# Optimization experiments

Measured on AMD Instinct MI355X. Metric: run time of the kernel, lower is better.

## Reference

```python
import jax, jax.numpy as jnp
import numpy as np

N0, N1, N2 = 80000, 40000, 20000
E1, E2 = 500000, 250000
FIN = 128        # in_channels
H = 2            # heads
C1 = 64          # hidden_channels -> layer1 out per head (concat -> 128)
C2 = 64          # out_channels -> layer2 out per head (mean over heads)
ED = 10          # edge_dim per embedding, total edge feat = 2*ED = 20
NTYPE, NTS = 23, 1158


def setup_inputs() -> dict:
    key = jax.random.key(0)
    ks = jax.random.split(key, 48)
    sc = 0.05
    inp = {
        "x": jax.random.normal(ks[0], (N0, FIN), jnp.float32),
        "ei1_src": jax.random.randint(ks[1], (E1,), 0, N0),
        "ei1_dst": jax.random.randint(ks[2], (E1,), 0, N1),
        "et1": jax.random.randint(ks[3], (E1,), 0, NTYPE),
        "ets1": jax.random.randint(ks[4], (E1,), 0, NTS),
        "ei2_src": jax.random.randint(ks[5], (E2,), 0, N1),
        "ei2_dst": jax.random.randint(ks[6], (E2,), 0, N2),
        "et2": jax.random.randint(ks[7], (E2,), 0, NTYPE),
        "ets2": jax.random.randint(ks[8], (E2,), 0, NTS),
        # shared edge embeddings (Linear(23,10), Linear(1158,10))
        "edge_W": jax.random.normal(ks[9], (ED, NTYPE), jnp.float32) * sc,
        "edge_b": jax.random.normal(ks[10], (ED,), jnp.float32) * sc,
        "time_W": jax.random.normal(ks[11], (ED, NTS), jnp.float32) * sc,
        "time_b": jax.random.normal(ks[12], (ED,), jnp.float32) * sc,
    }
    # layer 1: in=128, heads=2, C=64, concat=True (out dim 128)
    hc1 = H * C1
    inp["Wq1"] = jax.random.normal(ks[13], (hc1, FIN), jnp.float32) * sc
    inp["bq1"] = jnp.zeros((hc1,), jnp.float32)
    inp["Wk1"] = jax.random.normal(ks[14], (hc1, FIN), jnp.float32) * sc
    inp["bk1"] = jnp.zeros((hc1,), jnp.float32)
    inp["Wv1"] = jax.random.normal(ks[15], (hc1, FIN), jnp.float32) * sc
    inp["bv1"] = jnp.zeros((hc1,), jnp.float32)
    inp["We1"] = jax.random.normal(ks[16], (hc1, 2 * ED), jnp.float32) * sc
    inp["Wskip1"] = jax.random.normal(ks[17], (hc1, FIN), jnp.float32) * sc
    inp["bskip1"] = jnp.zeros((hc1,), jnp.float32)
    inp["Wbeta1"] = jax.random.normal(ks[18], (1, 3 * hc1), jnp.float32) * sc
    inp["ln_g"] = jnp.ones((hc1,), jnp.float32)
    inp["ln_b"] = jnp.zeros((hc1,), jnp.float32)
    # layer 2: in=128, heads=2, C=64, concat=False (out dim 64)
    hc2 = H * C2
    inp["Wq2"] = jax.random.normal(ks[19], (hc2, hc1), jnp.float32) * sc
    inp["bq2"] = jnp.zeros((hc2,), jnp.float32)
    inp["Wk2"] = jax.random.normal(ks[20], (hc2, hc1), jnp.float32) * sc
    inp["bk2"] = jnp.zeros((hc2,), jnp.float32)
    inp["Wv2"] = jax.random.normal(ks[21], (hc2, hc1), jnp.float32) * sc
    inp["bv2"] = jnp.zeros((hc2,), jnp.float32)
    inp["We2"] = jax.random.normal(ks[22], (hc2, 2 * ED), jnp.float32) * sc
    inp["Wskip2"] = jax.random.normal(ks[23], (C2, hc1), jnp.float32) * sc
    inp["bskip2"] = jnp.zeros((C2,), jnp.float32)
    inp["Wbeta2"] = jax.random.normal(ks[24], (1, 3 * C2), jnp.float32) * sc
    return inp


def _edge_feat(et, ets, edge_W, edge_b, time_W, time_b):
    # one_hot(e) @ W.T + b == W.T[e] + b (avoids materializing huge one-hot)
    return jnp.concatenate([jnp.take(edge_W.T, et, axis=0) + edge_b,
                            jnp.take(time_W.T, ets, axis=0) + time_b], axis=-1)


def _conv(x_src, x_dst, src, dst, ef, Wq, bq, Wk, bk, Wv, bv, We,
          Wskip, bskip, Wbeta, concat):
    n_dst = x_dst.shape[0]
    HC = Wq.shape[0]
    C = HC // H
    q = (x_dst @ Wq.T + bq).reshape(n_dst, H, C)            # [Nd,H,C]
    k = (x_src @ Wk.T + bk)[src].reshape(-1, H, C)          # [E,H,C]
    v = (x_src @ Wv.T + bv)[src].reshape(-1, H, C)
    e = (ef @ We.T).reshape(-1, H, C)
    k = k + e
    alpha = jnp.einsum('ehc,ehc->eh', q[dst], k) / np.sqrt(C).astype(np.float32)
    # segment softmax over destination nodes
    m = jax.ops.segment_max(alpha, dst, num_segments=n_dst)
    ex = jnp.exp(alpha - m[dst])
    s = jax.ops.segment_sum(ex, dst, num_segments=n_dst)
    a = ex / (s[dst] + 1e-16)                               # [E,H]
    msg = (v + e) * a[..., None]                            # [E,H,C]
    out = jax.ops.segment_sum(msg.reshape(-1, HC), dst, num_segments=n_dst)
    out = out if concat else out.reshape(n_dst, H, C).mean(axis=1)
    x_r = x_dst @ Wskip.T + bskip
    beta = jax.nn.sigmoid(
        jnp.concatenate([out, x_r, out - x_r], axis=-1) @ Wbeta.T)  # [Nd,1]
    return beta * x_r + (1.0 - beta) * out


def _layernorm(x, g, b):
    mu = x.mean(-1, keepdims=True)
    var = x.var(-1, keepdims=True)
    return (x - mu) / jnp.sqrt(var + 1e-5) * g + b


def reference(x, ei1_src, ei1_dst, et1, ets1, ei2_src, ei2_dst, et2, ets2,
              edge_W, edge_b, time_W, time_b,
              Wq1, bq1, Wk1, bk1, Wv1, bv1, We1, Wskip1, bskip1, Wbeta1,
              ln_g, ln_b,
              Wq2, bq2, Wk2, bk2, Wv2, bv2, We2, Wskip2, bskip2, Wbeta2):
    ef1 = _edge_feat(et1, ets1, edge_W, edge_b, time_W, time_b)
    h = _conv(x, x[:N1], ei1_src, ei1_dst, ef1,
              Wq1, bq1, Wk1, bk1, Wv1, bv1, We1, Wskip1, bskip1, Wbeta1,
              concat=True)
    h = jax.nn.gelu(_layernorm(h, ln_g, ln_b), approximate=False)
    ef2 = _edge_feat(et2, ets2, edge_W, edge_b, time_W, time_b)
    o = _conv(h, h[:N2], ei2_src, ei2_dst, ef2,
              Wq2, bq2, Wk2, bk2, Wv2, bv2, We2, Wskip2, bskip2, Wbeta2,
              concat=False)
    return jax.nn.log_softmax(o, axis=-1)
```

## Files before the change

kernel.cpp:

```cpp
#include <hip/hip_runtime.h>
#include <math.h>

#define N0 80000
#define N1 40000
#define N2 20000
#define E1C 500000
#define E2C 250000
#define NTYPE 23
#define NTS 1158

#define NB1 157
#define NB2 79
#define KV1B 1250
#define QR1B 625
#define CNTB 2930
#define KV2B 625
#define QR2B 313
#define FILLB 2930

#define OFF_XB    0u
#define OFF_QR1   5120000u
#define OFF_KV1   15360000u
#define OFF_H     25600000u
#define OFF_QR2   28160000u
#define OFF_KV2   32000000u
#define OFF_WB1   37120000u
#define OFF_BP1   37160000u
#define OFF_WB2   37170000u
#define OFF_BP2   37200000u
#define OFF_TA1   37210000u
#define OFF_TB1   37213000u
#define OFF_TA2   37370000u
#define OFF_TB2   37373000u
#define OFF_RP1   37530000u
#define OFF_CUR1  37580000u
#define OFF_EIX1  37630000u
#define OFF_BS1   38140000u
#define OFF_RP2   38150000u
#define OFF_CUR2  38180000u
#define OFF_EIX2  38210000u
#define OFF_BS2   38470000u
#define OFF_DONE  38480000u

typedef __bf16 bf16x8 __attribute__((ext_vector_type(8)));
typedef float f32x4 __attribute__((ext_vector_type(4)));

static __device__ __forceinline__ float b2f(unsigned short u) {
    union { unsigned int i; float f; } c;
    c.i = ((unsigned int)u) << 16;
    return c.f;
}
static __device__ __forceinline__ unsigned short f2b(float f) {
    unsigned int u = __float_as_uint(f);
    unsigned int r = (u + 0x7fffu + ((u >> 16) & 1u)) >> 16;
    return (unsigned short)r;
}
static __device__ __forceinline__ bf16x8 ldfrag(const unsigned short* p) {
    return *reinterpret_cast<const bf16x8*>(p);
}

template <int CTRL>
static __device__ __forceinline__ float dpp_addstep(float v) {
    int x = __builtin_amdgcn_mov_dpp(__float_as_int(v), CTRL, 0xF, 0xF, true);
    return v + __int_as_float(x);
}
static __device__ __forceinline__ float red16(float v) {
    v = dpp_addstep<0xB1>(v);
    v = dpp_addstep<0x4E>(v);
    v = dpp_addstep<0x141>(v);
    v = dpp_addstep<0x140>(v);
    return v;
}
template <int CTRL>
static __device__ __forceinline__ float dpp_maxstep(float v) {
    int x = __builtin_amdgcn_mov_dpp(__float_as_int(v), CTRL, 0xF, 0xF, true);
    return fmaxf(v, __int_as_float(x));
}
static __device__ __forceinline__ float red16max(float v) {
    v = dpp_maxstep<0xB1>(v);
    v = dpp_maxstep<0x4E>(v);
    v = dpp_maxstep<0x141>(v);
    v = dpp_maxstep<0x140>(v);
    return v;
}

#define LDSS 136

template <int NTILES>
static __device__ __forceinline__ void dev_gemm_bf16out(
    const unsigned short* __restrict__ XB, const unsigned short* __restrict__ WB,
    const float* __restrict__ BP, unsigned short* __restrict__ Y, int n, int blk,
    unsigned short* sb) {
    constexpr int COLS = NTILES * 16;
    constexpr int HALF = NTILES / 2;
    constexpr int HCOLS = HALF * 16;
    int wave = threadIdx.x >> 6, lane = threadIdx.x & 63;
    int m = lane & 15, quad = lane >> 4;
    int rowbase = blk * 64 + wave * 16;
    int arow = rowbase + m; if (arow >= n) arow = n - 1;
    unsigned short* swave = sb + wave * 16 * LDSS;
    const unsigned short* xrow = XB + (size_t)arow * 128 + quad * 8;
    bf16x8 a0 = ldfrag(xrow), a1 = ldfrag(xrow + 32);
    bf16x8 a2 = ldfrag(xrow + 64), a3 = ldfrag(xrow + 96);
    f32x4 acc[NTILES];
#pragma unroll
    for (int t = 0; t < NTILES; t++) acc[t] = (f32x4){0.f, 0.f, 0.f, 0.f};
#pragma unroll
    for (int t = 0; t < NTILES; t++) {
        const unsigned short* wt = WB + (size_t)t * 2048 + lane * 8;
        acc[t] = __builtin_amdgcn_mfma_f32_16x16x32_bf16(a0, ldfrag(wt), acc[t], 0, 0, 0);
        acc[t] = __builtin_amdgcn_mfma_f32_16x16x32_bf16(a1, ldfrag(wt + 512), acc[t], 0, 0, 0);
        acc[t] = __builtin_amdgcn_mfma_f32_16x16x32_bf16(a2, ldfrag(wt + 1024), acc[t], 0, 0, 0);
        acc[t] = __builtin_amdgcn_mfma_f32_16x16x32_bf16(a3, ldfrag(wt + 1536), acc[t], 0, 0, 0);
    }
    int tswz_bit = (quad >> 1) & 1;
#pragma unroll
    for (int half = 0; half < 2; half++) {
#pragma unroll
        for (int t = 0; t < HALF; t++) {
            int tt = half * HALF + t;
            int tsw = t ^ tswz_bit;
            float b = BP[tt * 16 + m];
#pragma unroll
            for (int r = 0; r < 4; r++)
                swave[(quad * 4 + r) * LDSS + tsw * 16 + m] = f2b(acc[tt][r] + b);
        }
#pragma unroll
        for (int i = 0; i < 4; i++) {
            int idx = i * 64 + lane;
            int r = idx / (HCOLS / 8), g = idx % (HCOLS / 8);
            int gs = g ^ (((r >> 3) & 1) << 1);
            int grow = rowbase + r;
            if (grow < n) {
                uint4 v = *(const uint4*)&swave[r * LDSS + gs * 8];
                *(uint4*)(Y + (size_t)grow * COLS + half * HCOLS + g * 8) = v;
            }
        }
    }
}

template <int NTILES>
static __device__ __forceinline__ void dev_gemm_f32out(
    const unsigned short* __restrict__ XB, const unsigned short* __restrict__ WB,
    const float* __restrict__ BP, float* __restrict__ Y, int n, int blk) {
    constexpr int COLS = NTILES * 16;
    int wave = threadIdx.x >> 6, lane = threadIdx.x & 63;
    int m = lane & 15, quad = lane >> 4;
    int rowbase = blk * 64 + wave * 16;
    int arow = rowbase + m; if (arow >= n) arow = n - 1;
    const unsigned short* xrow = XB + (size_t)arow * 128 + quad * 8;
    bf16x8 a0 = ldfrag(xrow), a1 = ldfrag(xrow + 32);
    bf16x8 a2 = ldfrag(xrow + 64), a3 = ldfrag(xrow + 96);
    f32x4 acc[NTILES];
#pragma unroll
    for (int t = 0; t < NTILES; t++) acc[t] = (f32x4){0.f, 0.f, 0.f, 0.f};
#pragma unroll
    for (int t = 0; t < NTILES; t++) {
        const unsigned short* wt = WB + (size_t)t * 2048 + lane * 8;
        acc[t] = __builtin_amdgcn_mfma_f32_16x16x32_bf16(a0, ldfrag(wt), acc[t], 0, 0, 0);
        acc[t] = __builtin_amdgcn_mfma_f32_16x16x32_bf16(a1, ldfrag(wt + 512), acc[t], 0, 0, 0);
        acc[t] = __builtin_amdgcn_mfma_f32_16x16x32_bf16(a2, ldfrag(wt + 1024), acc[t], 0, 0, 0);
        acc[t] = __builtin_amdgcn_mfma_f32_16x16x32_bf16(a3, ldfrag(wt + 1536), acc[t], 0, 0, 0);
    }
#pragma unroll
    for (int t = 0; t < NTILES; t++) {
        float b = BP[t * 16 + m];
#pragma unroll
        for (int r = 0; r < 4; r++) {
            int grow = rowbase + quad * 4 + r;
            if (grow < n) Y[(size_t)grow * COLS + t * 16 + m] = acc[t][r] + b;
        }
    }
}

__global__ __launch_bounds__(256) void prep(
    const float* __restrict__ x, unsigned short* __restrict__ XB,
    const float* __restrict__ Wk1, const float* __restrict__ Wv1,
    const float* __restrict__ Wq1, const float* __restrict__ Wskip1,
    const float* __restrict__ bk1, const float* __restrict__ bv1,
    const float* __restrict__ bq1, const float* __restrict__ bskip1,
    const float* __restrict__ Wk2, const float* __restrict__ Wv2,
    const float* __restrict__ Wq2, const float* __restrict__ Wskip2,
    const float* __restrict__ bk2, const float* __restrict__ bv2,
    const float* __restrict__ bq2, const float* __restrict__ bskip2,
    unsigned short* __restrict__ WB1, float* __restrict__ BP1,
    unsigned short* __restrict__ WB2, float* __restrict__ BP2,
    const float* __restrict__ edge_W, const float* __restrict__ edge_b,
    const float* __restrict__ time_W, const float* __restrict__ time_b,
    const float* __restrict__ We1, const float* __restrict__ We2,
    float* __restrict__ TA1, float* __restrict__ TB1,
    float* __restrict__ TA2, float* __restrict__ TB2,
    int* __restrict__ cnt1, int* __restrict__ cnt2, int* __restrict__ done) {
    int tid = blockIdx.x * blockDim.x + threadIdx.x;
    int stride = gridDim.x * blockDim.x;
    for (int i = tid; i < N0 * 32; i += stride) {
        float4 v = *(const float4*)(x + (size_t)i * 4);
        ushort4 u;
        u.x = f2b(v.x); u.y = f2b(v.y); u.z = f2b(v.z); u.w = f2b(v.w);
        *(ushort4*)(XB + (size_t)i * 4) = u;
    }
    for (int i = tid; i < 512 * 128; i += stride) {
        int j = i & 7, l = (i >> 3) & 63, ks = (i >> 9) & 3, t = i >> 11;
        int row = t * 16 + (l & 15);
        int col = ks * 32 + ((l >> 4) & 3) * 8 + j;
        const float* w; int off;
        if (row < 128) { w = Wk1; off = 0; }
        else if (row < 256) { w = Wv1; off = 128; }
        else if (row < 384) { w = Wq1; off = 256; }
        else { w = Wskip1; off = 384; }
        WB1[i] = f2b(w[(size_t)(row - off) * 128 + col]);
    }
    for (int i = tid; i < 512; i += stride) {
        const float* b; int off;
        if (i < 128) { b = bk1; off = 0; }
        else if (i < 256) { b = bv1; off = 128; }
        else if (i < 384) { b = bq1; off = 256; }
        else { b = bskip1; off = 384; }
        BP1[i] = b[i - off];
    }
    for (int i = tid; i < 448 * 128; i += stride) {
        int j = i & 7, l = (i >> 3) & 63, ks = (i >> 9) & 3, t = i >> 11;
        int row = t * 16 + (l & 15);
        int col = ks * 32 + ((l >> 4) & 3) * 8 + j;
        const float* w; int off;
        if (row < 128) { w = Wk2; off = 0; }
        else if (row < 256) { w = Wv2; off = 128; }
        else if (row < 384) { w = Wq2; off = 256; }
        else { w = Wskip2; off = 384; }
        WB2[i] = f2b(w[(size_t)(row - off) * 128 + col]);
    }
    for (int i = tid; i < 448; i += stride) {
        const float* b; int off;
        if (i < 128) { b = bk2; off = 0; }
        else if (i < 256) { b = bv2; off = 128; }
        else if (i < 384) { b = bq2; off = 256; }
        else { b = bskip2; off = 384; }
        BP2[i] = b[i - off];
    }
    const int TBL = (NTYPE + NTS) * 128;
    for (int i = tid; i < TBL; i += stride) {
        if (i < NTYPE * 128) {
            int e = i >> 7, c = i & 127;
            float s1 = 0.f, s2 = 0.f;
#pragma unroll
            for (int j = 0; j < 10; j++) {
                float fj = edge_W[j * NTYPE + e] + edge_b[j];
                s1 += fj * We1[c * 20 + j];
                s2 += fj * We2[c * 20 + j];
            }
            TA1[i] = s1; TA2[i] = s2;
        } else {
            int u = i - NTYPE * 128;
            int ts = u >> 7, c = u & 127;
            float s1 = 0.f, s2 = 0.f;
#pragma unroll
            for (int j = 0; j < 10; j++) {
                float fj = time_W[j * NTS + ts] + time_b[j];
                s1 += fj * We1[c * 20 + 10 + j];
                s2 += fj * We2[c * 20 + 10 + j];
            }
            TB1[u] = s1; TB2[u] = s2;
        }
    }
    for (int i = tid; i < N1 + N2 + 1; i += stride) {
        if (i < N1) cnt1[i] = 0;
        else if (i < N1 + N2) cnt2[i - N1] = 0;
        else *done = 0;
    }
}

__global__ __launch_bounds__(256) void mega_l1(
    const unsigned short* __restrict__ XB,
    const unsigned short* __restrict__ WB1, const float* __restrict__ BP1,
    unsigned short* __restrict__ KV1, float* __restrict__ QR1,
    const int* __restrict__ d1, const int* __restrict__ d2,
    int* __restrict__ cnt1, int* __restrict__ cnt2) {
    __shared__ unsigned short sbuf[4 * 16 * LDSS];
    int b = blockIdx.x;
    if (b < KV1B) {
        dev_gemm_bf16out<16>(XB, WB1, BP1, KV1, N0, b, sbuf);
    } else if (b < KV1B + QR1B) {
        dev_gemm_f32out<16>(XB, WB1 + 256 * 128, BP1 + 256, QR1, N1, b - KV1B);
    } else {
        int t = (b - KV1B - QR1B) * 256 + threadIdx.x;
        if (t < E1C) atomicAdd(&cnt1[d1[t]], 1);
        else {
            t -= E1C;
            if (t < E2C) atomicAdd(&cnt2[d2[t]], 1);
        }
    }
}

__global__ __launch_bounds__(256) void gemm_l2(
    const unsigned short* __restrict__ H,
    const unsigned short* __restrict__ WB2, const float* __restrict__ BP2,
    unsigned short* __restrict__ KV2, float* __restrict__ QR2) {
    __shared__ unsigned short sbuf[4 * 16 * LDSS];
    int b = blockIdx.x;
    if (b < KV2B) dev_gemm_bf16out<16>(H, WB2, BP2, KV2, N1, b, sbuf);
    else dev_gemm_f32out<12>(H, WB2 + 256 * 128, BP2 + 256, QR2, N2, b - KV2B);
}

__global__ __launch_bounds__(256) void bsum_scan(
    const int* __restrict__ cnt1, int* __restrict__ bs1,
    const int* __restrict__ cnt2, int* __restrict__ bs2, int* __restrict__ done) {
    __shared__ int s[256];
    __shared__ int amlast;
    int b = blockIdx.x;
    const int* cnt; int* bs; int n, lb;
    if (b < NB1) { cnt = cnt1; bs = bs1; n = N1; lb = b; }
    else { cnt = cnt2; bs = bs2; n = N2; lb = b - NB1; }
    int t = lb * 256 + threadIdx.x;
    s[threadIdx.x] = (t < n) ? cnt[t] : 0;
    __syncthreads();
    for (int off = 128; off; off >>= 1) {
        if (threadIdx.x < off) s[threadIdx.x] += s[threadIdx.x + off];
        __syncthreads();
    }
    if (threadIdx.x == 0) {
        atomicExch(&bs[lb], s[0]);
        __threadfence();
        int prev = atomicAdd(done, 1);
        amlast = (prev == NB1 + NB2 - 1) ? 1 : 0;
    }
    __syncthreads();
    if (!amlast) return;
    int tt = threadIdx.x;
    int v1 = (tt < NB1) ? atomicAdd(&bs1[tt], 0) : 0;
    s[tt] = v1;
    __syncthreads();
    for (int off = 1; off < 256; off <<= 1) {
        int u = (tt >= off) ? s[tt - off] : 0;
        __syncthreads();
        s[tt] += u;
        __syncthreads();
    }
    if (tt < NB1) bs1[tt] = s[tt] - v1;
    __syncthreads();
    int v2 = (tt < NB2) ? atomicAdd(&bs2[tt], 0) : 0;
    s[tt] = v2;
    __syncthreads();
    for (int off = 1; off < 256; off <<= 1) {
        int u = (tt >= off) ? s[tt - off] : 0;
        __syncthreads();
        s[tt] += u;
        __syncthreads();
    }
    if (tt < NB2) bs2[tt] = s[tt] - v2;
}

__global__ __launch_bounds__(256) void bscan_both(
    int* __restrict__ cnt1, const int* __restrict__ bs1, int* __restrict__ rp1,
    int* __restrict__ cnt2, const int* __restrict__ bs2, int* __restrict__ rp2) {
    __shared__ int s[256];
    int b = blockIdx.x;
    int* cnt; const int* bs; int* rp; int n, lb;
    if (b < NB1) { cnt = cnt1; bs = bs1; rp = rp1; n = N1; lb = b; }
    else { cnt = cnt2; bs = bs2; rp = rp2; n = N2; lb = b - NB1; }
    int t = lb * 256 + threadIdx.x;
    int v = (t < n) ? cnt[t] : 0;
    if (t < n) cnt[t] = 0;
    s[threadIdx.x] = v;
    __syncthreads();
    for (int off = 1; off < 256; off <<= 1) {
        int u = (threadIdx.x >= off) ? s[threadIdx.x - off] : 0;
        __syncthreads();
        s[threadIdx.x] += u;
        __syncthreads();
    }
    int incl = s[threadIdx.x];
    int base = bs[lb];
    if (t < n) rp[t] = base + incl - v;
    if (t == n - 1) rp[n] = base + incl;
}

__global__ __launch_bounds__(256) void fill_both(
    const int* __restrict__ d1, const int* __restrict__ rp1,
    int* __restrict__ cur1, int* __restrict__ eix1,
    const int* __restrict__ d2, const int* __restrict__ rp2,
    int* __restrict__ cur2, int* __restrict__ eix2) {
    int t = blockIdx.x * 256 + threadIdx.x;
    if (t < E1C) {
        int d = d1[t];
        eix1[rp1[d] + atomicAdd(&cur1[d], 1)] = t;
    } else {
        t -= E1C;
        if (t < E2C) {
            int d = d2[t];
            eix2[rp2[d] + atomicAdd(&cur2[d], 1)] = t;
        }
    }
}

__global__ __launch_bounds__(256) void agg_layer1(
    const int* __restrict__ rowptr, const int* __restrict__ eidx,
    const int* __restrict__ src, const int* __restrict__ et, const int* __restrict__ ets,
    const float* __restrict__ TA, const float* __restrict__ TB,
    const float* __restrict__ QR, const unsigned short* __restrict__ KV,
    const float* __restrict__ Wbeta,
    const float* __restrict__ ln_g, const float* __restrict__ ln_b,
    unsigned short* __restrict__ hout, int n) {
    int wid = (blockIdx.x * blockDim.x + threadIdx.x) >> 6;
    int lane = threadIdx.x & 63;
    if (wid >= n) return;
    int s = lane >> 5, cg = lane & 15;
    int co = ((lane >> 4) & 1) * 64 + 4 * cg;
    int beg = rowptr[wid], end = rowptr[wid + 1];
    float4 q4 = *(const float4*)(QR + (size_t)wid * 256 + co);
    float ax = 0.f, ay = 0.f, az = 0.f, aw = 0.f, suma = 0.f;
    int p = beg + s;
    if (p < end) {
        int e0 = eidx[p];
        int sn0 = src[e0], t0 = et[e0], ts0 = ets[e0];
        int p1 = p + 2;
        bool m1 = p1 < end;
        int e1 = eidx[m1 ? p1 : beg];
        int sn1 = src[e1], t1 = et[e1], ts1 = ets[e1];
        float4 ta0 = *(const float4*)(TA + t0 * 128 + co);
        float4 tb0 = *(const float4*)(TB + ts0 * 128 + co);
        const unsigned short* kv0 = KV + (size_t)sn0 * 256;
        ushort4 ku0 = *(const ushort4*)(kv0 + co);
        ushort4 vu0 = *(const ushort4*)(kv0 + 128 + co);
        for (;;) {
            int p2 = p1 + 2;
            bool m2 = p2 < end;
            int e2 = eidx[m2 ? p2 : beg];
            int sn2 = src[e2], t2 = et[e2], ts2 = ets[e2];
            float4 ta1 = *(const float4*)(TA + t1 * 128 + co);
            float4 tb1 = *(const float4*)(TB + ts1 * 128 + co);
            const unsigned short* kv1 = KV + (size_t)sn1 * 256;
            ushort4 ku1 = *(const ushort4*)(kv1 + co);
            ushort4 vu1 = *(const ushort4*)(kv1 + 128 + co);
            float e0c = ta0.x + tb0.x, e1c = ta0.y + tb0.y;
            float e2c = ta0.z + tb0.z, e3c = ta0.w + tb0.w;
            float pp = q4.x * (b2f(ku0.x) + e0c) + q4.y * (b2f(ku0.y) + e1c)
                     + q4.z * (b2f(ku0.z) + e2c) + q4.w * (b2f(ku0.w) + e3c);
            pp = red16(pp);
            float a = __expf(pp * 0.125f);
            ax += a * (b2f(vu0.x) + e0c); ay += a * (b2f(vu0.y) + e1c);
            az += a * (b2f(vu0.z) + e2c); aw += a * (b2f(vu0.w) + e3c);
            suma += a;
            if (!m1) break;
            p1 = p2; m1 = m2;
            sn1 = sn2; t1 = t2; ts1 = ts2;
            ta0 = ta1; tb0 = tb1; ku0 = ku1; vu0 = vu1;
        }
    }
    ax += __shfl_xor(ax, 32); ay += __shfl_xor(ay, 32);
    az += __shfl_xor(az, 32); aw += __shfl_xor(aw, 32);
    suma += __shfl_xor(suma, 32);
    float inv_s = 1.f / (suma + 1e-16f);
    float ox = ax * inv_s, oy = ay * inv_s, oz = az * inv_s, ow = aw * inv_s;
    float4 r4 = *(const float4*)(QR + (size_t)wid * 256 + 128 + co);
    float4 wo = *(const float4*)(Wbeta + co);
    float4 wr = *(const float4*)(Wbeta + 128 + co);
    float4 wd = *(const float4*)(Wbeta + 256 + co);
    float pb = wo.x * ox + wr.x * r4.x + wd.x * (ox - r4.x)
             + wo.y * oy + wr.y * r4.y + wd.y * (oy - r4.y)
             + wo.z * oz + wr.z * r4.z + wd.z * (oz - r4.z)
             + wo.w * ow + wr.w * r4.w + wd.w * (ow - r4.w);
    pb = red16(pb);
    pb += __shfl_xor(pb, 16);
    float beta = 1.f / (1.f + __expf(-pb));
    float gx = beta * r4.x + (1.f - beta) * ox;
    float gy = beta * r4.y + (1.f - beta) * oy;
    float gz = beta * r4.z + (1.f - beta) * oz;
    float gw = beta * r4.w + (1.f - beta) * ow;
    float sm = gx + gy + gz + gw;
    float sq = gx * gx + gy * gy + gz * gz + gw * gw;
    sm = red16(sm); sm += __shfl_xor(sm, 16);
    sq = red16(sq); sq += __shfl_xor(sq, 16);
    float mu = sm * (1.f / 128.f);
    float var = sq * (1.f / 128.f) - mu * mu;
    float inv = rsqrtf(var + 1e-5f);
    float4 lg = *(const float4*)(ln_g + co);
    float4 lb = *(const float4*)(ln_b + co);
    float yx = (gx - mu) * inv * lg.x + lb.x;
    float yy = (gy - mu) * inv * lg.y + lb.y;
    float yz = (gz - mu) * inv * lg.z + lb.z;
    float yw = (gw - mu) * inv * lg.w + lb.w;
    const float ISQ2 = 0.70710678118654752f;
    yx = 0.5f * yx * (1.f + erff(yx * ISQ2));
    yy = 0.5f * yy * (1.f + erff(yy * ISQ2));
    yz = 0.5f * yz * (1.f + erff(yz * ISQ2));
    yw = 0.5f * yw * (1.f + erff(yw * ISQ2));
    if (s == 0) {
        ushort4 hv;
        hv.x = f2b(yx); hv.y = f2b(yy); hv.z = f2b(yz); hv.w = f2b(yw);
        *(ushort4*)(hout + (size_t)wid * 128 + co) = hv;
    }
}

__global__ __launch_bounds__(256) void agg_layer2(
    const int* __restrict__ rowptr, const int* __restrict__ eidx,
    const int* __restrict__ src, const int* __restrict__ et, const int* __restrict__ ets,
    const float* __restrict__ TA, const float* __restrict__ TB,
    const float* __restrict__ QR, const unsigned short* __restrict__ KV,
    const float* __restrict__ Wbeta,
    float* __restrict__ o, int n) {
    int wid = (blockIdx.x * blockDim.x + threadIdx.x) >> 6;
    int lane = threadIdx.x & 63;
    if (wid >= n) return;
    int s = lane >> 5, cg = lane & 15;
    int co = ((lane >> 4) & 1) * 64 + 4 * cg;
    int beg = rowptr[wid], end = rowptr[wid + 1];
    float4 q4 = *(const float4*)(QR + (size_t)wid * 192 + co);
    float ax = 0.f, ay = 0.f, az = 0.f, aw = 0.f, suma = 0.f;
    int p = beg + s;
    if (p < end) {
        int e0 = eidx[p];
        int sn0 = src[e0], t0 = et[e0], ts0 = ets[e0];
        int p1 = p + 2;
        bool m1 = p1 < end;
        int e1 = eidx[m1 ? p1 : beg];
        int sn1 = src[e1], t1 = et[e1], ts1 = ets[e1];
        float4 ta0 = *(const float4*)(TA + t0 * 128 + co);
        float4 tb0 = *(const float4*)(TB + ts0 * 128 + co);
        const unsigned short* kv0 = KV + (size_t)sn0 * 256;
        ushort4 ku0 = *(const ushort4*)(kv0 + co);
        ushort4 vu0 = *(const ushort4*)(kv0 + 128 + co);
        for (;;) {
            int p2 = p1 + 2;
            bool m2 = p2 < end;
            int e2 = eidx[m2 ? p2 : beg];
            int sn2 = src[e2], t2 = et[e2], ts2 = ets[e2];
            float4 ta1 = *(const float4*)(TA + t1 * 128 + co);
            float4 tb1 = *(const float4*)(TB + ts1 * 128 + co);
            const unsigned short* kv1 = KV + (size_t)sn1 * 256;
            ushort4 ku1 = *(const ushort4*)(kv1 + co);
            ushort4 vu1 = *(const ushort4*)(kv1 + 128 + co);
            float e0c = ta0.x + tb0.x, e1c = ta0.y + tb0.y;
            float e2c = ta0.z + tb0.z, e3c = ta0.w + tb0.w;
            float pp = q4.x * (b2f(ku0.x) + e0c) + q4.y * (b2f(ku0.y) + e1c)
                     + q4.z * (b2f(ku0.z) + e2c) + q4.w * (b2f(ku0.w) + e3c);
            pp = red16(pp);
            float a = __expf(pp * 0.125f);
            ax += a * (b2f(vu0.x) + e0c); ay += a * (b2f(vu0.y) + e1c);
            az += a * (b2f(vu0.z) + e2c); aw += a * (b2f(vu0.w) + e3c);
            suma += a;
            if (!m1) break;
            p1 = p2; m1 = m2;
            sn1 = sn2; t1 = t2; ts1 = ts2;
            ta0 = ta1; tb0 = tb1; ku0 = ku1; vu0 = vu1;
        }
    }
    ax += __shfl_xor(ax, 32); ay += __shfl_xor(ay, 32);
    az += __shfl_xor(az, 32); aw += __shfl_xor(aw, 32);
    suma += __shfl_xor(suma, 32);
    float inv_s = 1.f / (suma + 1e-16f);
    float ox = ax * inv_s, oy = ay * inv_s, oz = az * inv_s, ow = aw * inv_s;
    ox = 0.5f * (ox + __shfl_xor(ox, 16));
    oy = 0.5f * (oy + __shfl_xor(oy, 16));
    oz = 0.5f * (oz + __shfl_xor(oz, 16));
    ow = 0.5f * (ow + __shfl_xor(ow, 16));
    float4 r4 = *(const float4*)(QR + (size_t)wid * 192 + 128 + 4 * cg);
    float4 wo = *(const float4*)(Wbeta + 4 * cg);
    float4 wr = *(const float4*)(Wbeta + 64 + 4 * cg);
    float4 wd = *(const float4*)(Wbeta + 128 + 4 * cg);
    float pb = wo.x * ox + wr.x * r4.x + wd.x * (ox - r4.x)
             + wo.y * oy + wr.y * r4.y + wd.y * (oy - r4.y)
             + wo.z * oz + wr.z * r4.z + wd.z * (oz - r4.z)
             + wo.w * ow + wr.w * r4.w + wd.w * (ow - r4.w);
    pb = red16(pb);
    float beta = 1.f / (1.f + __expf(-pb));
    float vx = beta * r4.x + (1.f - beta) * ox;
    float vy = beta * r4.y + (1.f - beta) * oy;
    float vz = beta * r4.z + (1.f - beta) * oz;
    float vw = beta * r4.w + (1.f - beta) * ow;
    float m = fmaxf(fmaxf(vx, vy), fmaxf(vz, vw));
    m = red16max(m);
    float se = __expf(vx - m) + __expf(vy - m) + __expf(vz - m) + __expf(vw - m);
    se = red16(se);
    float lse = m + logf(se);
    if (lane < 16)
        *(float4*)(o + (size_t)wid * 64 + 4 * cg) =
            make_float4(vx - lse, vy - lse, vz - lse, vw - lse);
}

extern "C" void kernel_launch(void* const* d_in, const int* in_sizes, int n_in,
                              void* d_out, int out_size, void* d_ws, size_t ws_size,
                              hipStream_t stream) {
    const float* x        = (const float*)d_in[0];
    const int*   ei1_src  = (const int*)d_in[1];
    const int*   ei1_dst  = (const int*)d_in[2];
    const int*   et1      = (const int*)d_in[3];
    const int*   ets1     = (const int*)d_in[4];
    const int*   ei2_src  = (const int*)d_in[5];
    const int*   ei2_dst  = (const int*)d_in[6];
    const int*   et2      = (const int*)d_in[7];
    const int*   ets2     = (const int*)d_in[8];
    const float* edge_W   = (const float*)d_in[9];
    const float* edge_b   = (const float*)d_in[10];
    const float* time_W   = (const float*)d_in[11];
    const float* time_b   = (const float*)d_in[12];
    const float* Wq1      = (const float*)d_in[13];
    const float* bq1      = (const float*)d_in[14];
    const float* Wk1      = (const float*)d_in[15];
    const float* bk1      = (const float*)d_in[16];
    const float* Wv1      = (const float*)d_in[17];
    const float* bv1      = (const float*)d_in[18];
    const float* We1      = (const float*)d_in[19];
    const float* Wskip1   = (const float*)d_in[20];
    const float* bskip1   = (const float*)d_in[21];
    const float* Wbeta1   = (const float*)d_in[22];
    const float* ln_g     = (const float*)d_in[23];
    const float* ln_b     = (const float*)d_in[24];
    const float* Wq2      = (const float*)d_in[25];
    const float* bq2      = (const float*)d_in[26];
    const float* Wk2      = (const float*)d_in[27];
    const float* bk2      = (const float*)d_in[28];
    const float* Wv2      = (const float*)d_in[29];
    const float* bv2      = (const float*)d_in[30];
    const float* We2      = (const float*)d_in[31];
    const float* Wskip2   = (const float*)d_in[32];
    const float* bskip2   = (const float*)d_in[33];
    const float* Wbeta2   = (const float*)d_in[34];

    float* ws = (float*)d_ws;
    unsigned short* xb  = (unsigned short*)(ws + OFF_XB);
    float* qr1          = ws + OFF_QR1;
    unsigned short* kv1 = (unsigned short*)(ws + OFF_KV1);
    unsigned short* h   = (unsigned short*)(ws + OFF_H);
    float* qr2          = ws + OFF_QR2;
    unsigned short* kv2 = (unsigned short*)(ws + OFF_KV2);
    unsigned short* wb1 = (unsigned short*)(ws + OFF_WB1);
    float* bp1          = ws + OFF_BP1;
    unsigned short* wb2 = (unsigned short*)(ws + OFF_WB2);
    float* bp2          = ws + OFF_BP2;
    float* ta1          = ws + OFF_TA1;
    float* tb1          = ws + OFF_TB1;
    float* ta2          = ws + OFF_TA2;
    float* tb2          = ws + OFF_TB2;
    int*   rp1          = (int*)(ws + OFF_RP1);
    int*   cur1         = (int*)(ws + OFF_CUR1);
    int*   eix1         = (int*)(ws + OFF_EIX1);
    int*   bs1          = (int*)(ws + OFF_BS1);
    int*   rp2          = (int*)(ws + OFF_RP2);
    int*   cur2         = (int*)(ws + OFF_CUR2);
    int*   eix2         = (int*)(ws + OFF_EIX2);
    int*   bs2          = (int*)(ws + OFF_BS2);
    int*   done         = (int*)(ws + OFF_DONE);

    prep<<<2048, 256, 0, stream>>>(
        x, xb,
        Wk1, Wv1, Wq1, Wskip1, bk1, bv1, bq1, bskip1,
        Wk2, Wv2, Wq2, Wskip2, bk2, bv2, bq2, bskip2,
        wb1, bp1, wb2, bp2,
        edge_W, edge_b, time_W, time_b, We1, We2,
        ta1, tb1, ta2, tb2, cur1, cur2, done);
    mega_l1<<<KV1B + QR1B + CNTB, 256, 0, stream>>>(
        xb, wb1, bp1, kv1, qr1, ei1_dst, ei2_dst, cur1, cur2);
    bsum_scan<<<NB1 + NB2, 256, 0, stream>>>(cur1, bs1, cur2, bs2, done);
    bscan_both<<<NB1 + NB2, 256, 0, stream>>>(cur1, bs1, rp1, cur2, bs2, rp2);
    fill_both<<<FILLB, 256, 0, stream>>>(ei1_dst, rp1, cur1, eix1,
                                         ei2_dst, rp2, cur2, eix2);
    agg_layer1<<<(N1 + 3) / 4, 256, 0, stream>>>(rp1, eix1, ei1_src, et1, ets1,
        ta1, tb1, qr1, kv1, Wbeta1, ln_g, ln_b, h, N1);
    gemm_l2<<<KV2B + QR2B, 256, 0, stream>>>(h, wb2, bp2, kv2, qr2);
    agg_layer2<<<(N2 + 3) / 4, 256, 0, stream>>>(rp2, eix2, ei2_src, et2, ets2,
        ta2, tb2, qr2, kv2, Wbeta2, (float*)d_out, N2);
}
```

Before: 401.3 us.

## Pack edge src/type/time into CSR-sorted records and fuse scan kernels

The fill kernel now writes a packed uint2 record (source node, edge type, timestamp index) in CSR order instead of an edge index. The aggregation kernels read these records with one contiguous 8-byte load, replacing an index load followed by three dependent scattered loads. The two scan kernels are merged into one that uses a grid-wide spin barrier on a done flag to wait for the block-sum scan, saving a launch. That barrier relies on all 236 blocks being resident at once, and the fill kernel now does extra scattered reads of src, et and ets.

Measured after the change: 392.4 us. -2.2%, faster.

```diff
diff --git a/kernel.cpp b/kernel.cpp
--- a/kernel.cpp
+++ b/kernel.cpp
@@ -34,13 +34,13 @@
 #define OFF_TB2   37373000u
 #define OFF_RP1   37530000u
 #define OFF_CUR1  37580000u
-#define OFF_EIX1  37630000u
-#define OFF_BS1   38140000u
-#define OFF_RP2   38150000u
-#define OFF_CUR2  38180000u
-#define OFF_EIX2  38210000u
-#define OFF_BS2   38470000u
-#define OFF_DONE  38480000u
+#define OFF_ED1   37630000u
+#define OFF_BS1   38640000u
+#define OFF_RP2   38650000u
+#define OFF_CUR2  38680000u
+#define OFF_ED2   38710000u
+#define OFF_BS2   39220000u
+#define OFF_DONE  39230000u
 
 typedef __bf16 bf16x8 __attribute__((ext_vector_type(8)));
 typedef float f32x4 __attribute__((ext_vector_type(4)));
@@ -262,10 +262,10 @@
             TB1[u] = s1; TB2[u] = s2;
         }
     }
-    for (int i = tid; i < N1 + N2 + 1; i += stride) {
+    for (int i = tid; i < N1 + N2 + 2; i += stride) {
         if (i < N1) cnt1[i] = 0;
         else if (i < N1 + N2) cnt2[i - N1] = 0;
-        else *done = 0;
+        else done[i - N1 - N2] = 0;
     }
 }
 
@@ -301,17 +301,19 @@
     else dev_gemm_f32out<12>(H, WB2 + 256 * 128, BP2 + 256, QR2, N2, b - KV2B);
 }
 
-__global__ __launch_bounds__(256) void bsum_scan(
-    const int* __restrict__ cnt1, int* __restrict__ bs1,
-    const int* __restrict__ cnt2, int* __restrict__ bs2, int* __restrict__ done) {
+__global__ __launch_bounds__(256) void csr_scan(
+    int* __restrict__ cnt1, int* __restrict__ bs1, int* __restrict__ rp1,
+    int* __restrict__ cnt2, int* __restrict__ bs2, int* __restrict__ rp2,
+    int* __restrict__ done) {
     __shared__ int s[256];
     __shared__ int amlast;
     int b = blockIdx.x;
-    const int* cnt; int* bs; int n, lb;
-    if (b < NB1) { cnt = cnt1; bs = bs1; n = N1; lb = b; }
-    else { cnt = cnt2; bs = bs2; n = N2; lb = b - NB1; }
+    int* cnt; int* bs; int* rp; int n, lb;
+    if (b < NB1) { cnt = cnt1; bs = bs1; rp = rp1; n = N1; lb = b; }
+    else { cnt = cnt2; bs = bs2; rp = rp2; n = N2; lb = b - NB1; }
     int t = lb * 256 + threadIdx.x;
-    s[threadIdx.x] = (t < n) ? cnt[t] : 0;
+    int v = (t < n) ? cnt[t] : 0;
+    s[threadIdx.x] = v;
     __syncthreads();
     for (int off = 128; off; off >>= 1) {
         if (threadIdx.x < off) s[threadIdx.x] += s[threadIdx.x + off];
@@ -320,46 +322,43 @@
     if (threadIdx.x == 0) {
         atomicExch(&bs[lb], s[0]);
         __threadfence();
-        int prev = atomicAdd(done, 1);
+        int prev = atomicAdd(&done[0], 1);
         amlast = (prev == NB1 + NB2 - 1) ? 1 : 0;
     }
     __syncthreads();
-    if (!amlast) return;
-    int tt = threadIdx.x;
-    int v1 = (tt < NB1) ? atomicAdd(&bs1[tt], 0) : 0;
-    s[tt] = v1;
+    if (amlast) {
+        int tt = threadIdx.x;
+        int v1 = (tt < NB1) ? atomicAdd(&bs1[tt], 0) : 0;
+        s[tt] = v1;
+        __syncthreads();
+        for (int off = 1; off < 256; off <<= 1) {
+            int u = (tt >= off) ? s[tt - off] : 0;
+            __syncthreads();
+            s[tt] += u;
+            __syncthreads();
+        }
+        if (tt < NB1) atomicExch(&bs1[tt], s[tt] - v1);
+        __syncthreads();
+        int v2 = (tt < NB2) ? atomicAdd(&bs2[tt], 0) : 0;
+        s[tt] = v2;
+        __syncthreads();
+        for (int off = 1; off < 256; off <<= 1) {
+            int u = (tt >= off) ? s[tt - off] : 0;
+            __syncthreads();
+            s[tt] += u;
+            __syncthreads();
+        }
+        if (tt < NB2) atomicExch(&bs2[tt], s[tt] - v2);
+        __threadfence();
+        __syncthreads();
+        if (tt == 0) atomicExch(&done[1], 1);
+    }
+    if (threadIdx.x == 0) {
+        while (atomicAdd(&done[1], 0) == 0) __builtin_amdgcn_s_sleep(1);
+    }
     __syncthreads();
-    for (int off = 1; off < 256; off <<= 1) {
-        int u = (tt >= off) ? s[tt - off] : 0;
-        __syncthreads();
-        s[tt] += u;
-        __syncthreads();
-    }
-    if (tt < NB1) bs1[tt] = s[tt] - v1;
-    __syncthreads();
-    int v2 = (tt < NB2) ? atomicAdd(&bs2[tt], 0) : 0;
-    s[tt] = v2;
-    __syncthreads();
-    for (int off = 1; off < 256; off <<= 1) {
-        int u = (tt >= off) ? s[tt - off] : 0;
-        __syncthreads();
-        s[tt] += u;
-        __syncthreads();
-    }
-    if (tt < NB2) bs2[tt] = s[tt] - v2;
-}
-
-__global__ __launch_bounds__(256) void bscan_both(
-    int* __restrict__ cnt1, const int* __restrict__ bs1, int* __restrict__ rp1,
-    int* __restrict__ cnt2, const int* __restrict__ bs2, int* __restrict__ rp2) {
-    __shared__ int s[256];
-    int b = blockIdx.x;
-    int* cnt; const int* bs; int* rp; int n, lb;
-    if (b < NB1) { cnt = cnt1; bs = bs1; rp = rp1; n = N1; lb = b; }
-    else { cnt = cnt2; bs = bs2; rp = rp2; n = N2; lb = b - NB1; }
-    int t = lb * 256 + threadIdx.x;
-    int v = (t < n) ? cnt[t] : 0;
-    if (t < n) cnt[t] = 0;
+    __threadfence();
+    int base = atomicAdd(&bs[lb], 0);
     s[threadIdx.x] = v;
     __syncthreads();
     for (int off = 1; off < 256; off <<= 1) {
@@ -369,32 +368,36 @@
         __syncthreads();
     }
     int incl = s[threadIdx.x];
-    int base = bs[lb];
-    if (t < n) rp[t] = base + incl - v;
+    if (t < n) { rp[t] = base + incl - v; cnt[t] = 0; }
     if (t == n - 1) rp[n] = base + incl;
 }
 
 __global__ __launch_bounds__(256) void fill_both(
-    const int* __restrict__ d1, const int* __restrict__ rp1,
-    int* __restrict__ cur1, int* __restrict__ eix1,
-    const int* __restrict__ d2, const int* __restrict__ rp2,
-    int* __restrict__ cur2, int* __restrict__ eix2) {
+    const int* __restrict__ d1, const int* __restrict__ s1,
+    const int* __restrict__ et1, const int* __restrict__ ets1,
+    const int* __restrict__ rp1, int* __restrict__ cur1, uint2* __restrict__ ed1,
+    const int* __restrict__ d2, const int* __restrict__ s2,
+    const int* __restrict__ et2, const int* __restrict__ ets2,
+    const int* __restrict__ rp2, int* __restrict__ cur2, uint2* __restrict__ ed2) {
     int t = blockIdx.x * 256 + threadIdx.x;
     if (t < E1C) {
         int d = d1[t];
-        eix1[rp1[d] + atomicAdd(&cur1[d], 1)] = t;
+        int pos = rp1[d] + atomicAdd(&cur1[d], 1);
+        ed1[pos] = make_uint2((unsigned)s1[t],
+                              (unsigned)(et1[t] | (ets1[t] << 16)));
     } else {
         t -= E1C;
         if (t < E2C) {
             int d = d2[t];
-            eix2[rp2[d] + atomicAdd(&cur2[d], 1)] = t;
+            int pos = rp2[d] + atomicAdd(&cur2[d], 1);
+            ed2[pos] = make_uint2((unsigned)s2[t],
+                                  (unsigned)(et2[t] | (ets2[t] << 16)));
         }
     }
 }
 
 __global__ __launch_bounds__(256) void agg_layer1(
-    const int* __restrict__ rowptr, const int* __restrict__ eidx,
-    const int* __restrict__ src, const int* __restrict__ et, const int* __restrict__ ets,
+    const int* __restrict__ rowptr, const uint2* __restrict__ ED,
     const float* __restrict__ TA, const float* __restrict__ TB,
     const float* __restrict__ QR, const unsigned short* __restrict__ KV,
     const float* __restrict__ Wbeta,
@@ -410,12 +413,11 @@
     float ax = 0.f, ay = 0.f, az = 0.f, aw = 0.f, suma = 0.f;
     int p = beg + s;
     if (p < end) {
-        int e0 = eidx[p];
-        int sn0 = src[e0], t0 = et[e0], ts0 = ets[e0];
+        uint2 d0 = ED[p];
         int p1 = p + 2;
         bool m1 = p1 < end;
-        int e1 = eidx[m1 ? p1 : beg];
-        int sn1 = src[e1], t1 = et[e1], ts1 = ets[e1];
+        uint2 dn = ED[m1 ? p1 : beg];
+        int sn0 = (int)d0.x, t0 = (int)(d0.y & 0xFFFF), ts0 = (int)(d0.y >> 16);
         float4 ta0 = *(const float4*)(TA + t0 * 128 + co);
         float4 tb0 = *(const float4*)(TB + ts0 * 128 + co);
         const unsigned short* kv0 = KV + (size_t)sn0 * 256;
@@ -424,8 +426,8 @@
         for (;;) {
             int p2 = p1 + 2;
             bool m2 = p2 < end;
-            int e2 = eidx[m2 ? p2 : beg];
-            int sn2 = src[e2], t2 = et[e2], ts2 = ets[e2];
+            uint2 dnn = ED[m2 ? p2 : beg];
+            int sn1 = (int)dn.x, t1 = (int)(dn.y & 0xFFFF), ts1 = (int)(dn.y >> 16);
             float4 ta1 = *(const float4*)(TA + t1 * 128 + co);
             float4 tb1 = *(const float4*)(TB + ts1 * 128 + co);
             const unsigned short* kv1 = KV + (size_t)sn1 * 256;
@@ -441,8 +443,7 @@
             az += a * (b2f(vu0.z) + e2c); aw += a * (b2f(vu0.w) + e3c);
             suma += a;
             if (!m1) break;
-            p1 = p2; m1 = m2;
-            sn1 = sn2; t1 = t2; ts1 = ts2;
+            p1 = p2; m1 = m2; dn = dnn;
             ta0 = ta1; tb0 = tb1; ku0 = ku1; vu0 = vu1;
         }
     }
@@ -492,8 +493,7 @@
 }
 
 __global__ __launch_bounds__(256) void agg_layer2(
-    const int* __restrict__ rowptr, const int* __restrict__ eidx,
-    const int* __restrict__ src, const int* __restrict__ et, const int* __restrict__ ets,
+    const int* __restrict__ rowptr, const uint2* __restrict__ ED,
     const float* __restrict__ TA, const float* __restrict__ TB,
     const float* __restrict__ QR, const unsigned short* __restrict__ KV,
     const float* __restrict__ Wbeta,
@@ -508,12 +508,11 @@
     float ax = 0.f, ay = 0.f, az = 0.f, aw = 0.f, suma = 0.f;
     int p = beg + s;
     if (p < end) {
-        int e0 = eidx[p];
-        int sn0 = src[e0], t0 = et[e0], ts0 = ets[e0];
+        uint2 d0 = ED[p];
         int p1 = p + 2;
         bool m1 = p1 < end;
-        int e1 = eidx[m1 ? p1 : beg];
-        int sn1 = src[e1], t1 = et[e1], ts1 = ets[e1];
+        uint2 dn = ED[m1 ? p1 : beg];
+        int sn0 = (int)d0.x, t0 = (int)(d0.y & 0xFFFF), ts0 = (int)(d0.y >> 16);
         float4 ta0 = *(const float4*)(TA + t0 * 128 + co);
         float4 tb0 = *(const float4*)(TB + ts0 * 128 + co);
         const unsigned short* kv0 = KV + (size_t)sn0 * 256;
@@ -522,8 +521,8 @@
         for (;;) {
             int p2 = p1 + 2;
             bool m2 = p2 < end;
-            int e2 = eidx[m2 ? p2 : beg];
-            int sn2 = src[e2], t2 = et[e2], ts2 = ets[e2];
+            uint2 dnn = ED[m2 ? p2 : beg];
+            int sn1 = (int)dn.x, t1 = (int)(dn.y & 0xFFFF), ts1 = (int)(dn.y >> 16);
             float4 ta1 = *(const float4*)(TA + t1 * 128 + co);
             float4 tb1 = *(const float4*)(TB + ts1 * 128 + co);
             const unsigned short* kv1 = KV + (size_t)sn1 * 256;
@@ -539,8 +538,7 @@
             az += a * (b2f(vu0.z) + e2c); aw += a * (b2f(vu0.w) + e3c);
             suma += a;
             if (!m1) break;
-            p1 = p2; m1 = m2;
-            sn1 = sn2; t1 = t2; ts1 = ts2;
+            p1 = p2; m1 = m2; dn = dnn;
             ta0 = ta1; tb0 = tb1; ku0 = ku1; vu0 = vu1;
         }
     }
@@ -633,11 +631,11 @@
     float* tb2          = ws + OFF_TB2;
     int*   rp1          = (int*)(ws + OFF_RP1);
     int*   cur1         = (int*)(ws + OFF_CUR1);
-    int*   eix1         = (int*)(ws + OFF_EIX1);
+    uint2* ed1          = (uint2*)(ws + OFF_ED1);
     int*   bs1          = (int*)(ws + OFF_BS1);
     int*   rp2          = (int*)(ws + OFF_RP2);
     int*   cur2         = (int*)(ws + OFF_CUR2);
-    int*   eix2         = (int*)(ws + OFF_EIX2);
+    uint2* ed2          = (uint2*)(ws + OFF_ED2);
     int*   bs2          = (int*)(ws + OFF_BS2);
     int*   done         = (int*)(ws + OFF_DONE);
 
@@ -650,13 +648,13 @@
         ta1, tb1, ta2, tb2, cur1, cur2, done);
     mega_l1<<<KV1B + QR1B + CNTB, 256, 0, stream>>>(
         xb, wb1, bp1, kv1, qr1, ei1_dst, ei2_dst, cur1, cur2);
-    bsum_scan<<<NB1 + NB2, 256, 0, stream>>>(cur1, bs1, cur2, bs2, done);
-    bscan_both<<<NB1 + NB2, 256, 0, stream>>>(cur1, bs1, rp1, cur2, bs2, rp2);
-    fill_both<<<FILLB, 256, 0, stream>>>(ei1_dst, rp1, cur1, eix1,
-                                         ei2_dst, rp2, cur2, eix2);
-    agg_layer1<<<(N1 + 3) / 4, 256, 0, stream>>>(rp1, eix1, ei1_src, et1, ets1,
+    csr_scan<<<NB1 + NB2, 256, 0, stream>>>(cur1, bs1, rp1, cur2, bs2, rp2, done);
+    fill_both<<<FILLB, 256, 0, stream>>>(
+        ei1_dst, ei1_src, et1, ets1, rp1, cur1, ed1,
+        ei2_dst, ei2_src, et2, ets2, rp2, cur2, ed2);
+    agg_layer1<<<(N1 + 3) / 4, 256, 0, stream>>>(rp1, ed1,
         ta1, tb1, qr1, kv1, Wbeta1, ln_g, ln_b, h, N1);
     gemm_l2<<<KV2B + QR2B, 256, 0, stream>>>(h, wb2, bp2, kv2, qr2);
-    agg_layer2<<<(N2 + 3) / 4, 256, 0, stream>>>(rp2, eix2, ei2_src, et2, ets2,
+    agg_layer2<<<(N2 + 3) / 4, 256, 0, stream>>>(rp2, ed2,
         ta2, tb2, qr2, kv2, Wbeta2, (float*)d_out, N2);
 }
```
